# Performance work log

Measured on AMD Instinct MI355X. Metric: run time of the kernel, lower is better.

The kernel has to match this reference:

```python
import jax, jax.numpy as jnp
import numpy as np

# ---- hyperparams from init_kwargs ----
WX, WY, WW, WH = 10.0, 10.0, 5.0, 5.0      # bbox_reg_weights
BBOX_XFORM_CLIP = float(np.log(1000.0 / 16.0))
SCORE_THRESH = 0.05
NMS_THRESH = 0.5
DETECTIONS_PER_IMG = 100
MIN_SIZE = 0.01


def decode_boxes(rel_codes, boxes):
    # torchvision BoxCoder.decode_single with weights (10,10,5,5)
    widths = boxes[:, 2] - boxes[:, 0]
    heights = boxes[:, 3] - boxes[:, 1]
    ctr_x = boxes[:, 0] + 0.5 * widths
    ctr_y = boxes[:, 1] + 0.5 * heights
    dx = rel_codes[:, 0] / WX
    dy = rel_codes[:, 1] / WY
    dw = jnp.minimum(rel_codes[:, 2] / WW, BBOX_XFORM_CLIP)
    dh = jnp.minimum(rel_codes[:, 3] / WH, BBOX_XFORM_CLIP)
    pcx = dx * widths + ctr_x
    pcy = dy * heights + ctr_y
    pw = jnp.exp(dw) * widths
    ph = jnp.exp(dh) * heights
    return jnp.stack([pcx - 0.5 * pw, pcy - 0.5 * ph,
                      pcx + 0.5 * pw, pcy + 0.5 * ph], axis=1)


def iou_one_vs_all(box, boxes):
    # torchvision box_iou of one box vs all boxes -> [N]
    area1 = (box[2] - box[0]) * (box[3] - box[1])
    area2 = (boxes[:, 2] - boxes[:, 0]) * (boxes[:, 3] - boxes[:, 1])
    lt = jnp.maximum(box[:2], boxes[:, :2])
    rb = jnp.minimum(box[2:], boxes[:, 2:])
    wh = jnp.clip(rb - lt, 0.0)
    inter = wh[:, 0] * wh[:, 1]
    return inter / (area1 + area2 - inter)


def postprocess(class_logits, box_regression, proposals, image_h, image_w):
    boxes = decode_boxes(box_regression, proposals)            # [N,4]
    scores = jax.nn.softmax(class_logits, axis=-1)             # [N,C]
    # clip_boxes_to_image: x in [0,W], y in [0,H]
    boxes = jnp.stack([jnp.clip(boxes[:, 0], 0.0, image_w),
                       jnp.clip(boxes[:, 1], 0.0, image_h),
                       jnp.clip(boxes[:, 2], 0.0, image_w),
                       jnp.clip(boxes[:, 3], 0.0, image_h)], axis=1)
    # top-1 class per anchor (argmax over all classes, as in the source)
    labels = jnp.argmax(scores, axis=1)                        # [N]
    top1 = jnp.take_along_axis(scores, labels[:, None], axis=1)[:, 0]
    # score threshold + remove_small_boxes -> mask instead of dynamic filter
    valid = ((top1 > SCORE_THRESH)
             & ((boxes[:, 2] - boxes[:, 0]) >= MIN_SIZE)
             & ((boxes[:, 3] - boxes[:, 1]) >= MIN_SIZE))
    masked_scores = jnp.where(valid, top1, -1.0)

    # per-class (batched) NMS: pick max-score box, suppress same-class overlaps
    def step(s, _):
        idx = jnp.argmax(s)
        best_score = s[idx]
        best_box = boxes[idx]
        best_lab = labels[idx]
        sup = (iou_one_vs_all(best_box, boxes) > NMS_THRESH) & (labels == best_lab)
        s = jnp.where(sup, -1.0, s).at[idx].set(-1.0)
        return s, (best_box, best_score, best_lab)

    _, (out_b, out_s, out_l) = jax.lax.scan(step, masked_scores, None,
                                            length=DETECTIONS_PER_IMG)
    v = out_s > 0.0                                            # pad slots -> score<=0
    out_b = jnp.where(v[:, None], out_b, 0.0)
    out_s = jnp.where(v, out_s, 0.0)
    out_l = jnp.where(v, out_l, -1)
    return out_b, out_s, out_l


def setup_inputs() -> dict:
    key = jax.random.key(0)
    k1, k2, k3, k4, k5, k6 = jax.random.split(key, 6)
    N, C = 200000, 91
    H, W = 512, 512
    class_logits = jax.random.normal(k1, (N, C), dtype=jnp.float32)
    box_regression = jax.random.normal(k2, (N, 4), dtype=jnp.float32)
    cx = jax.random.uniform(k3, (N,), dtype=jnp.float32) * W
    cy = jax.random.uniform(k4, (N,), dtype=jnp.float32) * H
    bw = jax.random.uniform(k5, (N,), dtype=jnp.float32) * 120.0 + 8.0
    bh = jax.random.uniform(k6, (N,), dtype=jnp.float32) * 120.0 + 8.0
    proposals = jnp.stack([cx - 0.5 * bw, cy - 0.5 * bh,
                           cx + 0.5 * bw, cy + 0.5 * bh], axis=1)
    return {"class_logits": class_logits, "box_regression": box_regression,
            "proposals": proposals, "image_h": H, "image_w": W}


def reference(class_logits, box_regression, proposals, image_h, image_w):
    return postprocess(class_logits, box_regression, proposals,
                       float(image_h), float(image_w))
```

## Files before the change

### kernel.cpp

```cpp
#include <hip/hip_runtime.h>

#define NBINS   1024
#define TARGETC 128
#define CAPW    192
#define DET     100
#define XCLIP   4.135166556742356f
#define CHUNK   48
#define TILE4   1152
#define TOPK    3
#define SCAP    64

__device__ inline float scalar_to_float(const int* p) {
  int v = *p;
  return (v >= 0 && v < (1 << 20)) ? (float)v : __int_as_float(v);
}

struct Box { float x1, y1, x2, y2; };

__device__ inline Box decode_clip(float4 r, float4 p, float W, float H) {
  float w = p.z - p.x, h = p.w - p.y;
  float cx = p.x + 0.5f * w, cy = p.y + 0.5f * h;
  float dx = r.x / 10.f, dy = r.y / 10.f;
  float dw = fminf(r.z / 5.f, XCLIP), dh = fminf(r.w / 5.f, XCLIP);
  float pcx = dx * w + cx, pcy = dy * h + cy;
  float pw = __expf(dw) * w, ph = __expf(dh) * h;
  Box b;
  b.x1 = fminf(fmaxf(pcx - 0.5f * pw, 0.f), W);
  b.y1 = fminf(fmaxf(pcy - 0.5f * ph, 0.f), H);
  b.x2 = fminf(fmaxf(pcx + 0.5f * pw, 0.f), W);
  b.y2 = fminf(fmaxf(pcy + 0.5f * ph, 0.f), H);
  return b;
}

__global__ __launch_bounds__(256) void k1_score(
    const float* __restrict__ logits, const float* __restrict__ reg,
    const float* __restrict__ prop, const int* __restrict__ ph,
    const int* __restrict__ pw, unsigned long long* __restrict__ buckets,
    int N) {
  __shared__ float4 tile[TILE4];
  __shared__ unsigned long long candS[SCAP];
  __shared__ int candN;
  const int t = threadIdx.x, wv = t >> 6, lane = t & 63;
  if (t == 0) candN = 0;
  if (t < SCAP) candS[t] = 0ULL;
  const float W = scalar_to_float(pw), H = scalar_to_float(ph);
  const int base = blockIdx.x * CHUNK;
  const int rows = (base < N) ? min(CHUNK, N - base) : 0;
  if (rows > 0) {
    const int nf = rows * 91, nf4 = nf >> 2;
    const float4* s4 = (const float4*)(logits + (size_t)base * 91);
    #pragma unroll
    for (int k = 0; k < 5; ++k) {
      int b4 = (wv + (k << 2)) << 6;
      if (b4 < nf4) {
        int g = b4 + lane;
        if (g > nf4 - 1) g = nf4 - 1;
        __builtin_amdgcn_global_load_lds(
            (const __attribute__((address_space(1))) void*)(s4 + g),
            (__attribute__((address_space(3))) void*)(&tile[0] + b4),
            16, 0, 0);
      }
    }
    for (int i = (nf4 << 2) + t; i < nf; i += 256)
      ((float*)tile)[i] = logits[(size_t)base * 91 + i];
  }
  __syncthreads();
  if (rows > 0) {
    const int r = t >> 2, s = t & 3;
    if (r < rows) {
      const float* rowp = (const float*)tile + r * 91;
      float mv = -3.402823466e38f; int mi = 1 << 20;
      float e0 = 0.f, e1 = 0.f;
      #pragma unroll
      for (int k = 0; k < 23; ++k) {
        int j = s + (k << 2);
        if (j < 91) {
          float v = rowp[j];
          float ex = __expf(v);
          if (k & 1) e1 += ex; else e0 += ex;
          if (v > mv) { mv = v; mi = j; }
        }
      }
      float e = e0 + e1;
      #pragma unroll
      for (int m = 1; m <= 2; m <<= 1) {
        float ov = __shfl_xor(mv, m, 64);
        int   oi = __shfl_xor(mi, m, 64);
        float oe = __shfl_xor(e, m, 64);
        e += oe;
        if (ov > mv || (ov == mv && oi < mi)) { mv = ov; mi = oi; }
      }
      if (s == 0) {
        float top1 = __expf(mv) / e;
        const int row = base + r;
        float4 rg = ((const float4*)reg)[row];
        float4 pp = ((const float4*)prop)[row];
        Box b = decode_clip(rg, pp, W, H);
        bool valid = (top1 > 0.05f) && ((b.x2 - b.x1) >= 0.01f) && ((b.y2 - b.y1) >= 0.01f);
        if (valid) {
          unsigned int low = ((0x1FFFFFFu - (unsigned int)row) << 7) |
                             (unsigned int)mi;
          unsigned long long key =
              ((unsigned long long)__float_as_uint(top1) << 32) |
              (unsigned long long)low;
          int pos = atomicAdd(&candN, 1);
          if (pos < SCAP) candS[pos] = key;
        }
      }
    }
  }
  __syncthreads();
  const int nc = (candN < SCAP) ? candN : SCAP;
  if (t < TOPK && t >= nc) buckets[(size_t)blockIdx.x * TOPK + t] = 0ULL;
  if (t < nc) {
    unsigned long long my = candS[t];
    int r = 0;
    const int ncr = (nc + 7) & ~7;
    #pragma unroll 8
    for (int j = 0; j < ncr; ++j) r += (candS[j] > my) ? 1 : 0;
    if (r < TOPK) buckets[(size_t)blockIdx.x * TOPK + r] = my;
  }
}

__global__ __launch_bounds__(1024) void k2_tail(
    const unsigned long long* __restrict__ buckets,
    const float* __restrict__ reg, const float* __restrict__ prop,
    const int* __restrict__ ph, const int* __restrict__ pw,
    float* __restrict__ out, int N, int nk2) {
  __shared__ unsigned int lh[4][NBINS];
  __shared__ unsigned long long keys[CAPW];
  __shared__ unsigned int wsum[16];
  __shared__ unsigned int wtail[16];
  __shared__ int bstar;
  __shared__ unsigned int gcnt;
  __shared__ float rx1[CAPW], ry1[CAPW], rx2[CAPW], ry2[CAPW], rsc[CAPW];
  __shared__ int rlab[CAPW];
  __shared__ unsigned int sup[CAPW * 6];
  __shared__ unsigned int colAny[6];
  __shared__ int keepL[DET];
  __shared__ int nkS;
  const int t = threadIdx.x;
  const int lane = t & 63, w = t >> 6;
  const ulonglong2* B2 = (const ulonglong2*)buckets;
  ulonglong2 v8[7];
  #pragma unroll
  for (int i = 0; i < 7; ++i) {
    int j = t + (i << 10);
    if (j < nk2) v8[i] = B2[j];
    else { v8[i].x = 0ULL; v8[i].y = 0ULL; }
  }
  for (int i = t; i < 4 * NBINS; i += 1024) ((unsigned int*)lh)[i] = 0u;
  if (t < CAPW) keys[t] = 0ULL;
  if (t < CAPW * 6 - 1024) sup[t + 1024] = 0u;
  sup[t < CAPW * 6 ? t : 0] = 0u;
  if (t < 6) colAny[t] = 0u;
  if (t == 0) { bstar = 0; gcnt = 0u; nkS = 0; }
  __syncthreads();
  const int sh = t & 3;
  #pragma unroll
  for (int i = 0; i < 7; ++i) {
    if (v8[i].x) {
      float s = __uint_as_float((unsigned int)(v8[i].x >> 32));
      int b = (int)(s * (float)NBINS);
      if (b > NBINS - 1) b = NBINS - 1;
      atomicAdd(&lh[sh][b], 1u);
    }
    if (v8[i].y) {
      float s = __uint_as_float((unsigned int)(v8[i].y >> 32));
      int b = (int)(s * (float)NBINS);
      if (b > NBINS - 1) b = NBINS - 1;
      atomicAdd(&lh[sh][b], 1u);
    }
  }
  __syncthreads();
  const unsigned int h0 = lh[0][t] + lh[1][t] + lh[2][t] + lh[3][t];
  unsigned int v = h0;
  #pragma unroll
  for (int m = 1; m < 64; m <<= 1) {
    unsigned int o = __shfl_down(v, m, 64);
    if (lane + m < 64) v += o;
  }
  if (lane == 0) wsum[w] = v;
  __syncthreads();
  if (w == 0) {
    unsigned int u = (lane < 16) ? wsum[lane] : 0u;
    unsigned int inc = u;
    #pragma unroll
    for (int m = 1; m < 16; m <<= 1) {
      unsigned int o = __shfl_down(inc, m, 64);
      if (lane + m < 16) inc += o;
    }
    if (lane < 16) wtail[lane] = inc - u;
  }
  __syncthreads();
  const unsigned int St = v + wtail[w];
  const unsigned int St1 = St - h0;
  if (St >= TARGETC && St1 < TARGETC) {
    int b = (St > CAPW) ? t + 1 : t;
    if (b > NBINS - 1) b = NBINS - 1;
    bstar = b;
  }
  __syncthreads();
  const int bs = bstar;
  #pragma unroll
  for (int i = 0; i < 7; ++i) {
    #pragma unroll
    for (int e = 0; e < 2; ++e) {
      unsigned long long key = e ? v8[i].y : v8[i].x;
      if (key) {
        float s = __uint_as_float((unsigned int)(key >> 32));
        int b = (int)(s * (float)NBINS);
        if (b > NBINS - 1) b = NBINS - 1;
        if (b >= bs) {
          unsigned int pos = atomicAdd(&gcnt, 1u);
          if (pos < CAPW) keys[pos] = key;
        }
      }
    }
  }
  __syncthreads();
  const int count = (gcnt < (unsigned int)CAPW) ? (int)gcnt : CAPW;
  const float W = scalar_to_float(pw), H = scalar_to_float(ph);
  if (t < CAPW) {
    unsigned long long my = keys[t];
    int r = 0;
    #pragma unroll 8
    for (int j = 0; j < CAPW; ++j) r += (keys[j] > my) ? 1 : 0;
    if (t < count) {
      unsigned int low = (unsigned int)(my & 0xFFFFFFFFULL);
      int lab = (int)(low & 127u);
      int idx = (int)(0x1FFFFFFu - (low >> 7));
      if (idx < 0) idx = 0;
      if (idx > N - 1) idx = N - 1;
      float4 rr = ((const float4*)reg)[idx];
      float4 pp = ((const float4*)prop)[idx];
      Box b = decode_clip(rr, pp, W, H);
      rx1[r] = b.x1; ry1[r] = b.y1; rx2[r] = b.x2; ry2[r] = b.y2;
      rsc[r] = __uint_as_float((unsigned int)(my >> 32));
      rlab[r] = lab;
    } else {
      rlab[t] = -1 - t;
      rx1[t] = 0.f; ry1[t] = 0.f; rx2[t] = 0.f; ry2[t] = 0.f; rsc[t] = 0.f;
    }
  }
  __syncthreads();
  #pragma unroll 4
  for (int p = t; p < (CAPW << 8); p += 1024) {
    int a = p >> 8, b = p & 255;
    if (a < b && b < CAPW && rlab[a] == rlab[b]) {
      float ax = fmaxf(rx1[a], rx1[b]), ay = fmaxf(ry1[a], ry1[b]);
      float bx = fminf(rx2[a], rx2[b]), by = fminf(ry2[a], ry2[b]);
      float iw = fmaxf(bx - ax, 0.f), ih = fmaxf(by - ay, 0.f);
      float inter = iw * ih;
      float a1 = (rx2[a] - rx1[a]) * (ry2[a] - ry1[a]);
      float a2 = (rx2[b] - rx1[b]) * (ry2[b] - ry1[b]);
      if (inter / (a1 + a2 - inter) > 0.5f) {
        atomicOr(&sup[b * 6 + (a >> 5)], 1u << (a & 31));
        atomicOr(&colAny[b >> 5], 1u << (b & 31));
      }
    }
  }
  __syncthreads();
  if (t == 0) {
    unsigned int K0 = 0, K1 = 0, K2 = 0, K3 = 0, K4 = 0, K5 = 0;
    int nk = 0;
#define RESOLVE_WORD(WI, KREG)                                          \
    if (nk < DET && (WI) * 32 < count) {                                \
      unsigned int anyw = colAny[WI];                                   \
      int lim = count - (WI) * 32; if (lim > 32) lim = 32;              \
      for (int b = 0; b < lim; ++b) {                                   \
        if (nk >= DET) break;                                           \
        int p = (WI) * 32 + b;                                          \
        bool keep;                                                      \
        if (!((anyw >> b) & 1u)) {                                      \
          keep = true;                                                  \
        } else {                                                        \
          const unsigned int* col = &sup[p * 6];                        \
          unsigned int hit = (col[0] & K0) | (col[1] & K1) |            \
                             (col[2] & K2) | (col[3] & K3) |            \
                             (col[4] & K4) | (col[5] & K5);             \
          keep = (hit == 0u);                                           \
        }                                                               \
        if (keep) { keepL[nk++] = p; KREG |= (1u << b); }               \
      }                                                                 \
    }
    RESOLVE_WORD(0, K0)
    RESOLVE_WORD(1, K1)
    RESOLVE_WORD(2, K2)
    RESOLVE_WORD(3, K3)
    RESOLVE_WORD(4, K4)
    RESOLVE_WORD(5, K5)
#undef RESOLVE_WORD
    nkS = nk;
  }
  __syncthreads();
  if (t < DET) {
    int nk = nkS;
    bool vld = t < nk;
    int p = vld ? keepL[t] : 0;
    out[t * 4 + 0] = vld ? rx1[p] : 0.f;
    out[t * 4 + 1] = vld ? ry1[p] : 0.f;
    out[t * 4 + 2] = vld ? rx2[p] : 0.f;
    out[t * 4 + 3] = vld ? ry2[p] : 0.f;
    out[400 + t] = vld ? rsc[p] : 0.f;
    out[500 + t] = vld ? (float)rlab[p] : -1.f;
  }
}

extern "C" void kernel_launch(void* const* d_in, const int* in_sizes, int n_in,
                              void* d_out, int out_size, void* d_ws, size_t ws_size,
                              hipStream_t stream) {
  const float* logits = (const float*)d_in[0];
  const float* reg    = (const float*)d_in[1];
  const float* prop   = (const float*)d_in[2];
  const int*   ph     = (const int*)d_in[3];
  const int*   pw     = (const int*)d_in[4];
  float* out = (float*)d_out;

  const int N = in_sizes[1] / 4;
  const int grid = (((N + CHUNK - 1) / CHUNK) + 1) & ~1;
  const int nk2 = grid * TOPK / 2;

  unsigned long long* buckets = (unsigned long long*)d_ws;

  k1_score<<<grid, 256, 0, stream>>>(logits, reg, prop, ph, pw, buckets, N);
  k2_tail<<<1, 1024, 0, stream>>>(buckets, reg, prop, ph, pw, out, N, nk2);
}
```

Baseline: 44.12 us.

## Process one row per thread with direct register loads instead of LDS staging

The score kernel no longer stages 48-row chunks of logits into LDS with four threads per row. Each thread now loads its whole 91-float row straight into 24 float4 registers, handles the unaligned start with a per-element mask, and computes the softmax sum and argmax itself. Blocks now cover 256 rows, so the per-block top-K rises to 6 and the candidate buffer to 256 entries, which also changes the size of the tail kernel's input. The cost is uncoalesced strided global loads, a large register footprint with occupancy pinned by launch_bounds(256,1), and many more candidates in the per-block rank sort.

```diff
diff --git a/kernel.cpp b/kernel.cpp
--- a/kernel.cpp
+++ b/kernel.cpp
@@ -5,10 +5,8 @@
 #define CAPW    192
 #define DET     100
 #define XCLIP   4.135166556742356f
-#define CHUNK   48
-#define TILE4   1152
-#define TOPK    3
-#define SCAP    64
+#define TOPK    6
+#define SCAP    256
 
 __device__ inline float scalar_to_float(const int* p) {
   int v = *p;
@@ -32,81 +30,85 @@
   return b;
 }
 
-__global__ __launch_bounds__(256) void k1_score(
+__global__ __launch_bounds__(256, 1) void k1_score(
     const float* __restrict__ logits, const float* __restrict__ reg,
     const float* __restrict__ prop, const int* __restrict__ ph,
     const int* __restrict__ pw, unsigned long long* __restrict__ buckets,
     int N) {
-  __shared__ float4 tile[TILE4];
   __shared__ unsigned long long candS[SCAP];
   __shared__ int candN;
-  const int t = threadIdx.x, wv = t >> 6, lane = t & 63;
+  const int t = threadIdx.x;
   if (t == 0) candN = 0;
-  if (t < SCAP) candS[t] = 0ULL;
+  candS[t] = 0ULL;
+  __syncthreads();
   const float W = scalar_to_float(pw), H = scalar_to_float(ph);
-  const int base = blockIdx.x * CHUNK;
-  const int rows = (base < N) ? min(CHUNK, N - base) : 0;
-  if (rows > 0) {
-    const int nf = rows * 91, nf4 = nf >> 2;
-    const float4* s4 = (const float4*)(logits + (size_t)base * 91);
-    #pragma unroll
-    for (int k = 0; k < 5; ++k) {
-      int b4 = (wv + (k << 2)) << 6;
-      if (b4 < nf4) {
-        int g = b4 + lane;
-        if (g > nf4 - 1) g = nf4 - 1;
-        __builtin_amdgcn_global_load_lds(
-            (const __attribute__((address_space(1))) void*)(s4 + g),
-            (__attribute__((address_space(3))) void*)(&tile[0] + b4),
-            16, 0, 0);
+  const int row = blockIdx.x * 256 + t;
+  if (row < N) {
+    float mv0 = -3.402823466e38f, mv1 = -3.402823466e38f;
+    int   mi0 = 1 << 20,          mi1 = 1 << 20;
+    float e0 = 0.f, e1 = 0.f;
+    if (row < N - 1) {
+      const size_t a = (size_t)row * 91;
+      const float4* b4 = (const float4*)(logits + (a & ~(size_t)3));
+      const int shift = (int)(a & 3);
+      float4 R[24];
+      #pragma unroll
+      for (int j = 0; j < 24; ++j) R[j] = b4[j];
+      #pragma unroll
+      for (int j = 0; j < 24; ++j) {
+        {
+          int idx = 4 * j + 0 - shift;
+          bool ok = (idx >= 0) & (idx < 91);
+          float ex = __expf(R[j].x);
+          e0 += ok ? ex : 0.f;
+          if (ok && R[j].x > mv0) { mv0 = R[j].x; mi0 = idx; }
+        }
+        {
+          int idx = 4 * j + 1 - shift;
+          bool ok = (idx >= 0) & (idx < 91);
+          float ex = __expf(R[j].y);
+          e1 += ok ? ex : 0.f;
+          if (ok && R[j].y > mv1) { mv1 = R[j].y; mi1 = idx; }
+        }
+        {
+          int idx = 4 * j + 2 - shift;
+          bool ok = (idx >= 0) & (idx < 91);
+          float ex = __expf(R[j].z);
+          e0 += ok ? ex : 0.f;
+          if (ok && R[j].z > mv0) { mv0 = R[j].z; mi0 = idx; }
+        }
+        {
+          int idx = 4 * j + 3 - shift;
+          bool ok = (idx >= 0) & (idx < 91);
+          float ex = __expf(R[j].w);
+          e1 += ok ? ex : 0.f;
+          if (ok && R[j].w > mv1) { mv1 = R[j].w; mi1 = idx; }
+        }
       }
-    }
-    for (int i = (nf4 << 2) + t; i < nf; i += 256)
-      ((float*)tile)[i] = logits[(size_t)base * 91 + i];
-  }
-  __syncthreads();
-  if (rows > 0) {
-    const int r = t >> 2, s = t & 3;
-    if (r < rows) {
-      const float* rowp = (const float*)tile + r * 91;
-      float mv = -3.402823466e38f; int mi = 1 << 20;
-      float e0 = 0.f, e1 = 0.f;
-      #pragma unroll
-      for (int k = 0; k < 23; ++k) {
-        int j = s + (k << 2);
-        if (j < 91) {
-          float v = rowp[j];
-          float ex = __expf(v);
-          if (k & 1) e1 += ex; else e0 += ex;
-          if (v > mv) { mv = v; mi = j; }
-        }
+    } else {
+      const float* rp = logits + (size_t)row * 91;
+      for (int j = 0; j < 91; ++j) {
+        float v = rp[j];
+        float ex = __expf(v);
+        if (j & 1) { e1 += ex; if (v > mv1) { mv1 = v; mi1 = j; } }
+        else       { e0 += ex; if (v > mv0) { mv0 = v; mi0 = j; } }
       }
-      float e = e0 + e1;
-      #pragma unroll
-      for (int m = 1; m <= 2; m <<= 1) {
-        float ov = __shfl_xor(mv, m, 64);
-        int   oi = __shfl_xor(mi, m, 64);
-        float oe = __shfl_xor(e, m, 64);
-        e += oe;
-        if (ov > mv || (ov == mv && oi < mi)) { mv = ov; mi = oi; }
-      }
-      if (s == 0) {
-        float top1 = __expf(mv) / e;
-        const int row = base + r;
-        float4 rg = ((const float4*)reg)[row];
-        float4 pp = ((const float4*)prop)[row];
-        Box b = decode_clip(rg, pp, W, H);
-        bool valid = (top1 > 0.05f) && ((b.x2 - b.x1) >= 0.01f) && ((b.y2 - b.y1) >= 0.01f);
-        if (valid) {
-          unsigned int low = ((0x1FFFFFFu - (unsigned int)row) << 7) |
-                             (unsigned int)mi;
-          unsigned long long key =
-              ((unsigned long long)__float_as_uint(top1) << 32) |
-              (unsigned long long)low;
-          int pos = atomicAdd(&candN, 1);
-          if (pos < SCAP) candS[pos] = key;
-        }
-      }
+    }
+    float mv = mv0; int mi = mi0;
+    if (mv1 > mv || (mv1 == mv && mi1 < mi)) { mv = mv1; mi = mi1; }
+    float top1 = __expf(mv) / (e0 + e1);
+    float4 rg = ((const float4*)reg)[row];
+    float4 pp = ((const float4*)prop)[row];
+    Box b = decode_clip(rg, pp, W, H);
+    bool valid = (top1 > 0.05f) && ((b.x2 - b.x1) >= 0.01f) && ((b.y2 - b.y1) >= 0.01f);
+    if (valid) {
+      unsigned int low = ((0x1FFFFFFu - (unsigned int)row) << 7) |
+                         (unsigned int)mi;
+      unsigned long long key =
+          ((unsigned long long)__float_as_uint(top1) << 32) |
+          (unsigned long long)low;
+      int pos = atomicAdd(&candN, 1);
+      if (pos < SCAP) candS[pos] = key;
     }
   }
   __syncthreads();
@@ -318,8 +320,8 @@
   float* out = (float*)d_out;
 
   const int N = in_sizes[1] / 4;
-  const int grid = (((N + CHUNK - 1) / CHUNK) + 1) & ~1;
-  const int nk2 = grid * TOPK / 2;
+  const int grid = (N + 255) / 256;
+  const int nk2 = (grid * TOPK + 1) / 2;
 
   unsigned long long* buckets = (unsigned long long*)d_ws;
 
```

Measured after the change: 58.30 us. 1.32x slower.
